# Kernel optimization log

Measured on AMD Instinct MI355X. Metric: run time of the kernel, lower is better.

## Reference

```python
import jax, jax.numpy as jnp
import numpy as np

# Config mirrors init_kwargs
D_IN, D_OUT, HEADS, SEQ, BATCH = 1024, 64, 16, 2048, 2


def setup_inputs() -> dict:
    key = jax.random.key(0)
    kx, kq, kk, kv = jax.random.split(key, 4)
    scale = 1.0 / np.sqrt(D_IN)
    x = jax.random.normal(kx, (BATCH, SEQ, D_IN), dtype=jnp.float32)
    # Stacked per-head projection weights, [H, d_in, d_out] (qkv_bias=False)
    Wq = jax.random.normal(kq, (HEADS, D_IN, D_OUT), dtype=jnp.float32) * scale
    Wk = jax.random.normal(kk, (HEADS, D_IN, D_OUT), dtype=jnp.float32) * scale
    Wv = jax.random.normal(kv, (HEADS, D_IN, D_OUT), dtype=jnp.float32) * scale
    return {"x": x, "Wq": Wq, "Wk": Wk, "Wv": Wv}


def reference(x, Wq, Wk, Wv):
    # x: [B, S, d_in]; W*: [H, d_in, d_out]
    q = jnp.einsum("bsd,hde->bhse", x, Wq)
    k = jnp.einsum("bsd,hde->bhse", x, Wk)
    v = jnp.einsum("bsd,hde->bhse", x, Wv)
    scores = jnp.einsum("bhse,bhte->bhst", q, k) / jnp.sqrt(
        jnp.asarray(D_OUT, dtype=q.dtype)
    )
    S = x.shape[1]
    causal = jnp.tril(jnp.ones((S, S), dtype=bool))  # [S, S]
    scores = jnp.where(causal[None, None], scores, -jnp.inf)
    attn = jax.nn.softmax(scores, axis=-1)  # dropout=0.0 (eval)
    ctx = jnp.einsum("bhst,bhte->bhse", attn, v)  # [B, H, S, d_out]
    # concat heads on last dim -> [B, S, H*d_out]
    B, H, S2, E = ctx.shape
    return jnp.transpose(ctx, (0, 2, 1, 3)).reshape(B, S2, H * E)
```

## Files before the change

kernel.cpp:

```cpp
#include <hip/hip_runtime.h>
#include <hip/hip_bf16.h>
#include <math.h>

#define BATCH 2
#define SEQ   2048
#define DIN   1024
#define HEADS 16
#define EDIM  64

#define NX   (BATCH*SEQ*DIN)
#define NW   (3*HEADS*DIN*EDIM)
#define NQKV (BATCH*HEADS*SEQ*EDIM)

#define QSCALE 0.18033688011112042f

typedef __attribute__((ext_vector_type(8))) short short8;
typedef __attribute__((ext_vector_type(4))) float f32x4;

static __device__ __forceinline__ ushort f2bf(float f) {
    __hip_bfloat16 h = __float2bfloat16(f);
    return *reinterpret_cast<ushort*>(&h);
}
static __device__ __forceinline__ float bf2f(ushort u) {
    uint v = (uint)u << 16;
    return *reinterpret_cast<float*>(&v);
}

static __device__ __forceinline__ void gload16(const void* g, void* l) {
    void* gv = const_cast<void*>(g);
    __builtin_amdgcn_global_load_lds(
        (__attribute__((address_space(1))) void*)gv,
        (__attribute__((address_space(3))) void*)l,
        16, 0, 0);
}

static __device__ __forceinline__ void barrier_fenced() {
    asm volatile("" ::: "memory");
    __builtin_amdgcn_s_barrier();
    asm volatile("" ::: "memory");
}

__constant__ int FT_IT[24]  = {15,15, 7,14,14,13,13, 6,12,12,11,11, 5,10,10, 9, 9, 4, 8, 8, 3, 2, 1, 0};
__constant__ int FT_K0[24]  = { 0,16, 0, 0,15, 0,14, 0, 0,13, 0,12, 0, 0,11, 0,10, 0, 0, 9, 0, 0, 0, 0};
__constant__ int FT_CNT[24] = {16,16,16,15,15,14,14,14,13,13,12,12,12,11,11,10,10,10, 9, 9, 8, 6, 4, 2};
__constant__ int FT_SL[24]  = {14,15,-1,12,13,10,11,-1, 8, 9, 6, 7,-1, 4, 5, 2, 3,-1, 0, 1,-1,-1,-1,-1};

__global__ __launch_bounds__(256) void prep(
    const float* __restrict__ x, const float* __restrict__ Wq,
    const float* __restrict__ Wk, const float* __restrict__ Wv,
    ushort* __restrict__ xb, ushort* __restrict__ wt)
{
    const int t = threadIdx.x;
    if (blockIdx.x < 1024) {
        const int v0 = blockIdx.x * 256 + t;
#pragma unroll
        for (int i = 0; i < 4; ++i) {
            int i4 = (v0 + i * 262144) * 4;
            float4 f = *(const float4*)(x + i4);
            ushort4 o;
            o.x = f2bf(f.x); o.y = f2bf(f.y); o.z = f2bf(f.z); o.w = f2bf(f.w);
            *(ushort4*)(xb + i4) = o;
        }
    } else {
        const int bid = blockIdx.x - 1024;
        const int dt  = bid & 15;
        const int h   = (bid >> 4) & 15;
        const int mat = bid >> 8;

        const float* W = (mat == 0) ? Wq : (mat == 1) ? Wk : Wv;
        const float* src = W + ((size_t)h * DIN + dt * 64) * EDIM;
        ushort* dst = wt + ((size_t)(mat * HEADS + h) * EDIM) * DIN + dt * 64;

        __shared__ ushort T[64][68];
#pragma unroll
        for (int i = 0; i < 16; ++i) {
            int v = t + i * 256;
            int d = v >> 6, e = v & 63;
            T[d][e] = f2bf(src[(size_t)d * EDIM + e]);
        }
        __syncthreads();
#pragma unroll
        for (int i = 0; i < 4; ++i) {
            int v = t + i * 256;
            int e = v >> 4, d4 = (v & 15) << 2;
            ushort4 ov;
            ov.x = T[d4 + 0][e]; ov.y = T[d4 + 1][e];
            ov.z = T[d4 + 2][e]; ov.w = T[d4 + 3][e];
            *(ushort4*)&dst[(size_t)e * DIN + d4] = ov;
        }
    }
}

__global__ __launch_bounds__(256) void qkv_gemm(
    const ushort* __restrict__ xb, const ushort* __restrict__ wt,
    ushort* __restrict__ qkv)
{
    const int bid = blockIdx.x;
    const int xcd = bid & 7;
    const int idx = bid >> 3;
    const int mt  = (xcd >> 1) * 8 + idx / 12;
    const int nt  = (xcd & 1) * 12 + idx % 12;
    const int m0 = mt * 128, n0 = nt * 128;
    const int b  = mt >> 4;

    __shared__ ushort As[2][128][64];
    __shared__ ushort Bs[2][128][64];

    const int t    = threadIdx.x;
    const int lane = t & 63;
    const int w    = t >> 6;
    const int wr   = w >> 1, wc = w & 1;
    const int fr   = lane & 15;
    const int fk   = (lane >> 4) * 8;
    const int rg   = (lane >> 4) * 4;
    const int sw   = (fr & 7) << 3;

    const ushort* xbase = xb + (size_t)m0 * DIN;
    const ushort* wbase = wt + (size_t)n0 * DIN;

    const int lrow = lane >> 3;
    const int lcol = ((lane & 7) ^ (lane >> 3)) << 3;

#define STAGE(buf, k0)                                                          \
    {                                                                           \
        _Pragma("unroll")                                                       \
        for (int j = 0; j < 4; ++j) {                                           \
            const int c = w * 4 + j;                                            \
            gload16(&xbase[(size_t)(c * 8 + lrow) * DIN + (k0) + lcol], &As[buf][c * 8][0]); \
            gload16(&wbase[(size_t)(c * 8 + lrow) * DIN + (k0) + lcol], &Bs[buf][c * 8][0]); \
        }                                                                       \
    }

    f32x4 acc[4][4];
#pragma unroll
    for (int i = 0; i < 4; ++i)
#pragma unroll
        for (int j = 0; j < 4; ++j) acc[i][j] = (f32x4)0.f;

    STAGE(0, 0);
    STAGE(1, 64);

    short8 a[4][2], bfr[4][2];

#define LOAD_FRAGS(cur)                                                         \
    {                                                                           \
        _Pragma("unroll")                                                       \
        for (int rb = 0; rb < 4; ++rb)                                          \
            _Pragma("unroll")                                                   \
            for (int kk = 0; kk < 2; ++kk) {                                    \
                a[rb][kk]   = *(const short8*)&As[cur][wr * 64 + rb * 16 + fr][(kk * 32 + fk) ^ sw]; \
                bfr[rb][kk] = *(const short8*)&Bs[cur][wc * 64 + rb * 16 + fr][(kk * 32 + fk) ^ sw]; \
            }                                                                   \
    }

#define DO_MFMA()                                                               \
    {                                                                           \
        _Pragma("unroll")                                                       \
        for (int kk = 0; kk < 2; ++kk)                                          \
            _Pragma("unroll")                                                   \
            for (int rb = 0; rb < 4; ++rb)                                      \
                _Pragma("unroll")                                               \
                for (int cf = 0; cf < 4; ++cf)                                  \
                    acc[rb][cf] = __builtin_amdgcn_mfma_f32_16x16x32_bf16(a[rb][kk], bfr[cf][kk], acc[rb][cf], 0, 0, 0); \
    }

    for (int kt = 0; kt < 15; ++kt) {
        const int cur = kt & 1;

        asm volatile("s_waitcnt vmcnt(8)" ::: "memory");
        __builtin_amdgcn_sched_barrier(0);
        barrier_fenced();

        LOAD_FRAGS(cur);

        asm volatile("s_waitcnt lgkmcnt(0)" ::: "memory");
        __builtin_amdgcn_sched_barrier(0);
        barrier_fenced();

        if (kt <= 13) STAGE(cur, (kt + 2) * 64);

        DO_MFMA();
    }
    {
        asm volatile("s_waitcnt vmcnt(0)" ::: "memory");
        __builtin_amdgcn_sched_barrier(0);
        barrier_fenced();
        LOAD_FRAGS(1);
        DO_MFMA();
    }
#undef STAGE
#undef LOAD_FRAGS
#undef DO_MFMA

    const int hg  = nt * 2 + wc;
    const int mat = hg >> 4;
    const int h   = hg & 15;
    const int s0  = (m0 & 2047) + wr * 64;
    if (mat < 2) {
        const float sc = (mat == 0) ? QSCALE : 1.0f;
        ushort* dst = qkv + (size_t)mat * NQKV
                    + ((size_t)((b * HEADS + h) * SEQ) + s0) * EDIM;
#pragma unroll
        for (int rb = 0; rb < 4; ++rb)
#pragma unroll
            for (int cf = 0; cf < 4; ++cf)
#pragma unroll
                for (int i = 0; i < 4; ++i)
                    dst[(size_t)(rb * 16 + rg + i) * EDIM + cf * 16 + fr] = f2bf(acc[rb][cf][i] * sc);
    } else {
        ushort* vtb = qkv + (size_t)2 * NQKV + ((size_t)(b * HEADS + h) * EDIM) * SEQ;
#pragma unroll
        for (int rb = 0; rb < 4; ++rb)
#pragma unroll
            for (int cf = 0; cf < 4; ++cf) {
                ushort4 ov;
                ov.x = f2bf(acc[rb][cf][0]); ov.y = f2bf(acc[rb][cf][1]);
                ov.z = f2bf(acc[rb][cf][2]); ov.w = f2bf(acc[rb][cf][3]);
                *(ushort4*)&vtb[(size_t)(cf * 16 + fr) * SEQ + s0 + rb * 16 + rg] = ov;
            }
    }
}

__global__ __launch_bounds__(512) void flash_part(
    const ushort* __restrict__ q, const ushort* __restrict__ k,
    const ushort* __restrict__ vt, float* __restrict__ out,
    ushort* __restrict__ pO, float* __restrict__ pl)
{
    const int bid  = blockIdx.x;
    const int item = bid >> 5;
    const int bh   = bid & 31;
    const int b    = bh >> 4;
    const int h    = bh & 15;
    const int it   = FT_IT[item];
    const int k0t  = FT_K0[item];
    const int cnt  = FT_CNT[item];
    const int slot = FT_SL[item];

    const ushort* Qb  = q  + ((size_t)((b * HEADS + h) * SEQ) + it * 128) * EDIM;
    const ushort* Kb  = k  + ((size_t)((b * HEADS + h) * SEQ)) * EDIM;
    const ushort* Vtb = vt + ((size_t)((b * HEADS + h) * EDIM)) * SEQ;

    __shared__ ushort Ks_[2][64][64];
    __shared__ ushort Vs_[2][64][64];
    __shared__ ushort Ps_[8][16][72];

    const int t    = threadIdx.x;
    const int lane = t & 63;
    const int w    = t >> 6;
    const int fr   = lane & 15;
    const int fk   = (lane >> 4) * 8;
    const int rg   = (lane >> 4) * 4;
    const int sw   = (fr & 7) << 3;

    const int srow8 = lane >> 3;
    const int sunit = (lane & 7) ^ srow8;

#define FSTAGE(buf, tile)                                                      \
    {                                                                          \
        gload16(&Kb[(size_t)((tile) * 64 + w * 8 + srow8) * EDIM + sunit * 8], \
                &Ks_[buf][w * 8][0]);                                          \
        gload16(&Vtb[(size_t)(w * 8 + srow8) * SEQ + (tile) * 64 + sunit * 8], \
                &Vs_[buf][w * 8][0]);                                          \
    }

    const int wrow0 = it * 128 + w * 16;
    const int lastT = wrow0 >> 6;
    const int qrow  = wrow0 + fr;

    short8 qf[2];
#pragma unroll
    for (int kk = 0; kk < 2; ++kk)
        qf[kk] = *(const short8*)&Qb[(size_t)(w * 16 + fr) * EDIM + kk * 32 + fk];
    asm volatile("s_waitcnt vmcnt(0)" ::: "memory");
    __builtin_amdgcn_sched_barrier(0);

    f32x4 o_[4];
#pragma unroll
    for (int cf = 0; cf < 4; ++cf) o_[cf] = (f32x4)0.f;
    float lpart = 0.f;

    FSTAGE(0, k0t);

    for (int ktl = 0; ktl < cnt; ++ktl) {
        const int cur  = ktl & 1;
        const int kt_g = k0t + ktl;

        asm volatile("s_waitcnt vmcnt(0)" ::: "memory");
        __builtin_amdgcn_sched_barrier(0);
        barrier_fenced();

        if (ktl + 1 < cnt) FSTAGE(cur ^ 1, k0t + ktl + 1);

        if (kt_g <= lastT) {
            f32x4 s[4];
#pragma unroll
            for (int cf = 0; cf < 4; ++cf) s[cf] = (f32x4)0.f;
#pragma unroll
            for (int cf = 0; cf < 4; ++cf)
#pragma unroll
                for (int kk = 0; kk < 2; ++kk) {
                    short8 kf = *(const short8*)&Ks_[cur][cf * 16 + fr][(kk * 32 + fk) ^ sw];
                    s[cf] = __builtin_amdgcn_mfma_f32_16x16x32_bf16(kf, qf[kk], s[cf], 0, 0, 0);
                }

            if (kt_g == lastT) {
#pragma unroll
                for (int cf = 0; cf < 4; ++cf)
#pragma unroll
                    for (int i = 0; i < 4; ++i) {
                        int kpos = kt_g * 64 + cf * 16 + rg + i;
                        if (kpos > qrow) s[cf][i] = -1e30f;
                    }
            }

            float ls = 0.f;
#pragma unroll
            for (int cf = 0; cf < 4; ++cf) {
                float p0 = __builtin_amdgcn_exp2f(s[cf][0]);
                float p1 = __builtin_amdgcn_exp2f(s[cf][1]);
                float p2 = __builtin_amdgcn_exp2f(s[cf][2]);
                float p3 = __builtin_amdgcn_exp2f(s[cf][3]);
                ls += (p0 + p1) + (p2 + p3);
                uint2 pk;
                pk.x = (uint)f2bf(p0) | ((uint)f2bf(p1) << 16);
                pk.y = (uint)f2bf(p2) | ((uint)f2bf(p3) << 16);
                *(uint2*)&Ps_[w][fr][cf * 16 + rg] = pk;
            }
            lpart += ls;

            short8 pf[2];
#pragma unroll
            for (int kb = 0; kb < 2; ++kb)
                pf[kb] = *(const short8*)&Ps_[w][fr][kb * 32 + fk];
#pragma unroll
            for (int cf = 0; cf < 4; ++cf)
#pragma unroll
                for (int kb = 0; kb < 2; ++kb) {
                    short8 vf = *(const short8*)&Vs_[cur][cf * 16 + fr][(kb * 32 + fk) ^ sw];
                    o_[cf] = __builtin_amdgcn_mfma_f32_16x16x32_bf16(vf, pf[kb], o_[cf], 0, 0, 0);
                }
        }
    }
#undef FSTAGE

    float ls = lpart;
    ls += __shfl_xor(ls, 16);
    ls += __shfl_xor(ls, 32);

    if (slot < 0) {
        const float inv = 1.f / ls;
        float* rowp = out + ((size_t)(b * SEQ + qrow)) * (HEADS * EDIM) + h * EDIM;
#pragma unroll
        for (int cf = 0; cf < 4; ++cf) {
            f32x4 ov = o_[cf] * inv;
            *(f32x4*)&rowp[cf * 16 + rg] = ov;
        }
    } else {
        ushort* po = pO + (((size_t)bh * 16 + slot) * 128 + (w * 16 + fr)) * 64;
#pragma unroll
        for (int cf = 0; cf < 4; ++cf) {
            ushort4 ov;
            ov.x = f2bf(o_[cf][0]); ov.y = f2bf(o_[cf][1]);
            ov.z = f2bf(o_[cf][2]); ov.w = f2bf(o_[cf][3]);
            *(ushort4*)&po[cf * 16 + rg] = ov;
        }
        if ((lane >> 4) == 0)
            pl[((size_t)bh * 16 + slot) * 128 + (w * 16 + fr)] = ls;
    }
}

__global__ __launch_bounds__(256) void combine(
    const ushort* __restrict__ pO, const float* __restrict__ pl,
    float* __restrict__ out)
{
    const int bid = blockIdx.x;
    const int bh  = bid & 31;
    const int b   = bh >> 4;
    const int h   = bh & 15;
    const int it8 = bid >> 5;
    const int it  = 8 + it8;

    const ushort* p0 = pO + ((size_t)bh * 16 + it8 * 2) * (128 * 64);
    const ushort* p1 = p0 + 128 * 64;
    const float*  l0 = pl + ((size_t)bh * 16 + it8 * 2) * 128;
    const float*  l1 = l0 + 128;

    const int t  = threadIdx.x;
    const int rr = t >> 6;
    const int e  = t & 63;

    for (int rb = 0; rb < 32; ++rb) {
        int row = rb * 4 + rr;
        float l = l0[row] + l1[row];
        float o = bf2f(p0[row * 64 + e]) + bf2f(p1[row * 64 + e]);
        out[((size_t)(b * SEQ + it * 128 + row)) * (HEADS * EDIM) + h * EDIM + e] = o / l;
    }
}

extern "C" void kernel_launch(void* const* d_in, const int* in_sizes, int n_in,
                              void* d_out, int out_size, void* d_ws, size_t ws_size,
                              hipStream_t stream) {
    const float* x  = (const float*)d_in[0];
    const float* Wq = (const float*)d_in[1];
    const float* Wk = (const float*)d_in[2];
    const float* Wv = (const float*)d_in[3];
    float* out = (float*)d_out;

    ushort* xb  = (ushort*)d_ws;
    ushort* wt  = xb + NX;
    ushort* qkv = wt + NW;
    ushort* pO  = qkv + (size_t)3 * NQKV;
    float*  pl  = (float*)(pO + (size_t)32 * 16 * 128 * 64);

    prep<<<1792, 256, 0, stream>>>(x, Wq, Wk, Wv, xb, wt);
    qkv_gemm<<<768, 256, 0, stream>>>(xb, wt, qkv);
    flash_part<<<768, 512, 0, stream>>>(
        qkv, qkv + NQKV, qkv + (size_t)2 * NQKV, out, pO, pl);
    combine<<<256, 256, 0, stream>>>(pO, pl, out);
}
```

Baseline: 81.43 us.

## Give each flash-attention wave two 16-row query tiles, halving block size

The flash_part kernel now runs 4 waves of 64 threads per block instead of 8. Each wave handles 32 query rows as two 16-row sub-tiles (A and B), so every K and V fragment read from shared memory feeds twice as many MFMAs. This cuts LDS read traffic per unit of math and halves the number of waves doing staging and barriers per block. In exchange, accumulator and score register use per wave roughly doubles, and fewer waves per block means less latency hiding unless occupancy rises.

```diff
diff --git a/kernel.cpp b/kernel.cpp
--- a/kernel.cpp
+++ b/kernel.cpp
@@ -221,7 +221,7 @@
     }
 }
 
-__global__ __launch_bounds__(512) void flash_part(
+__global__ __launch_bounds__(256) void flash_part(
     const ushort* __restrict__ q, const ushort* __restrict__ k,
     const ushort* __restrict__ vt, float* __restrict__ out,
     ushort* __restrict__ pO, float* __restrict__ pl)
@@ -242,7 +242,7 @@
 
     __shared__ ushort Ks_[2][64][64];
     __shared__ ushort Vs_[2][64][64];
-    __shared__ ushort Ps_[8][16][72];
+    __shared__ ushort Ps_[4][32][72];
 
     const int t    = threadIdx.x;
     const int lane = t & 63;
@@ -255,29 +255,36 @@
     const int srow8 = lane >> 3;
     const int sunit = (lane & 7) ^ srow8;
 
-#define FSTAGE(buf, tile)                                                      \
-    {                                                                          \
-        gload16(&Kb[(size_t)((tile) * 64 + w * 8 + srow8) * EDIM + sunit * 8], \
-                &Ks_[buf][w * 8][0]);                                          \
-        gload16(&Vtb[(size_t)(w * 8 + srow8) * SEQ + (tile) * 64 + sunit * 8], \
-                &Vs_[buf][w * 8][0]);                                          \
-    }
-
-    const int wrow0 = it * 128 + w * 16;
+#define FSTAGE(buf, tile)                                                        \
+    {                                                                            \
+        gload16(&Kb[(size_t)((tile) * 64 + w * 16 + srow8) * EDIM + sunit * 8],  \
+                &Ks_[buf][w * 16][0]);                                           \
+        gload16(&Kb[(size_t)((tile) * 64 + w * 16 + 8 + srow8) * EDIM + sunit * 8], \
+                &Ks_[buf][w * 16 + 8][0]);                                       \
+        gload16(&Vtb[(size_t)(w * 16 + srow8) * SEQ + (tile) * 64 + sunit * 8],  \
+                &Vs_[buf][w * 16][0]);                                           \
+        gload16(&Vtb[(size_t)(w * 16 + 8 + srow8) * SEQ + (tile) * 64 + sunit * 8], \
+                &Vs_[buf][w * 16 + 8][0]);                                       \
+    }
+
+    const int wrow0 = it * 128 + w * 32;
     const int lastT = wrow0 >> 6;
-    const int qrow  = wrow0 + fr;
-
-    short8 qf[2];
-#pragma unroll
-    for (int kk = 0; kk < 2; ++kk)
-        qf[kk] = *(const short8*)&Qb[(size_t)(w * 16 + fr) * EDIM + kk * 32 + fk];
+    const int qrowA = wrow0 + fr;
+    const int qrowB = wrow0 + 16 + fr;
+
+    short8 qfA[2], qfB[2];
+#pragma unroll
+    for (int kk = 0; kk < 2; ++kk) {
+        qfA[kk] = *(const short8*)&Qb[(size_t)(w * 32 + fr) * EDIM + kk * 32 + fk];
+        qfB[kk] = *(const short8*)&Qb[(size_t)(w * 32 + 16 + fr) * EDIM + kk * 32 + fk];
+    }
     asm volatile("s_waitcnt vmcnt(0)" ::: "memory");
     __builtin_amdgcn_sched_barrier(0);
 
-    f32x4 o_[4];
-#pragma unroll
-    for (int cf = 0; cf < 4; ++cf) o_[cf] = (f32x4)0.f;
-    float lpart = 0.f;
+    f32x4 oA[4], oB[4];
+#pragma unroll
+    for (int cf = 0; cf < 4; ++cf) { oA[cf] = (f32x4)0.f; oB[cf] = (f32x4)0.f; }
+    float lpA = 0.f, lpB = 0.f;
 
     FSTAGE(0, k0t);
 
@@ -292,16 +299,18 @@
         if (ktl + 1 < cnt) FSTAGE(cur ^ 1, k0t + ktl + 1);
 
         if (kt_g <= lastT) {
-            f32x4 s[4];
-#pragma unroll
-            for (int cf = 0; cf < 4; ++cf) s[cf] = (f32x4)0.f;
-#pragma unroll
-            for (int cf = 0; cf < 4; ++cf)
-#pragma unroll
-                for (int kk = 0; kk < 2; ++kk) {
-                    short8 kf = *(const short8*)&Ks_[cur][cf * 16 + fr][(kk * 32 + fk) ^ sw];
-                    s[cf] = __builtin_amdgcn_mfma_f32_16x16x32_bf16(kf, qf[kk], s[cf], 0, 0, 0);
-                }
+            f32x4 sA[4], sB[4];
+#pragma unroll
+            for (int cf = 0; cf < 4; ++cf) { sA[cf] = (f32x4)0.f; sB[cf] = (f32x4)0.f; }
+#pragma unroll
+            for (int cf = 0; cf < 4; ++cf) {
+                short8 kf0 = *(const short8*)&Ks_[cur][cf * 16 + fr][(fk) ^ sw];
+                short8 kf1 = *(const short8*)&Ks_[cur][cf * 16 + fr][(32 + fk) ^ sw];
+                sA[cf] = __builtin_amdgcn_mfma_f32_16x16x32_bf16(kf0, qfA[0], sA[cf], 0, 0, 0);
+                sA[cf] = __builtin_amdgcn_mfma_f32_16x16x32_bf16(kf1, qfA[1], sA[cf], 0, 0, 0);
+                sB[cf] = __builtin_amdgcn_mfma_f32_16x16x32_bf16(kf0, qfB[0], sB[cf], 0, 0, 0);
+                sB[cf] = __builtin_amdgcn_mfma_f32_16x16x32_bf16(kf1, qfB[1], sB[cf], 0, 0, 0);
+            }
 
             if (kt_g == lastT) {
 #pragma unroll
@@ -309,63 +318,87 @@
 #pragma unroll
                     for (int i = 0; i < 4; ++i) {
                         int kpos = kt_g * 64 + cf * 16 + rg + i;
-                        if (kpos > qrow) s[cf][i] = -1e30f;
+                        if (kpos > qrowA) sA[cf][i] = -1e30f;
+                        if (kpos > qrowB) sB[cf][i] = -1e30f;
                     }
             }
 
-            float ls = 0.f;
+            float lsA = 0.f, lsB = 0.f;
 #pragma unroll
             for (int cf = 0; cf < 4; ++cf) {
-                float p0 = __builtin_amdgcn_exp2f(s[cf][0]);
-                float p1 = __builtin_amdgcn_exp2f(s[cf][1]);
-                float p2 = __builtin_amdgcn_exp2f(s[cf][2]);
-                float p3 = __builtin_amdgcn_exp2f(s[cf][3]);
-                ls += (p0 + p1) + (p2 + p3);
-                uint2 pk;
-                pk.x = (uint)f2bf(p0) | ((uint)f2bf(p1) << 16);
-                pk.y = (uint)f2bf(p2) | ((uint)f2bf(p3) << 16);
-                *(uint2*)&Ps_[w][fr][cf * 16 + rg] = pk;
+                float a0 = __builtin_amdgcn_exp2f(sA[cf][0]);
+                float a1 = __builtin_amdgcn_exp2f(sA[cf][1]);
+                float a2 = __builtin_amdgcn_exp2f(sA[cf][2]);
+                float a3 = __builtin_amdgcn_exp2f(sA[cf][3]);
+                lsA += (a0 + a1) + (a2 + a3);
+                uint2 pka;
+                pka.x = (uint)f2bf(a0) | ((uint)f2bf(a1) << 16);
+                pka.y = (uint)f2bf(a2) | ((uint)f2bf(a3) << 16);
+                *(uint2*)&Ps_[w][fr][cf * 16 + rg] = pka;
+                float b0 = __builtin_amdgcn_exp2f(sB[cf][0]);
+                float b1 = __builtin_amdgcn_exp2f(sB[cf][1]);
+                float b2 = __builtin_amdgcn_exp2f(sB[cf][2]);
+                float b3 = __builtin_amdgcn_exp2f(sB[cf][3]);
+                lsB += (b0 + b1) + (b2 + b3);
+                uint2 pkb;
+                pkb.x = (uint)f2bf(b0) | ((uint)f2bf(b1) << 16);
+                pkb.y = (uint)f2bf(b2) | ((uint)f2bf(b3) << 16);
+                *(uint2*)&Ps_[w][16 + fr][cf * 16 + rg] = pkb;
             }
-            lpart += ls;
-
-            short8 pf[2];
-#pragma unroll
-            for (int kb = 0; kb < 2; ++kb)
-                pf[kb] = *(const short8*)&Ps_[w][fr][kb * 32 + fk];
-#pragma unroll
-            for (int cf = 0; cf < 4; ++cf)
-#pragma unroll
-                for (int kb = 0; kb < 2; ++kb) {
-                    short8 vf = *(const short8*)&Vs_[cur][cf * 16 + fr][(kb * 32 + fk) ^ sw];
-                    o_[cf] = __builtin_amdgcn_mfma_f32_16x16x32_bf16(vf, pf[kb], o_[cf], 0, 0, 0);
-                }
+            lpA += lsA;
+            lpB += lsB;
+
+            short8 pfA0 = *(const short8*)&Ps_[w][fr][fk];
+            short8 pfA1 = *(const short8*)&Ps_[w][fr][32 + fk];
+            short8 pfB0 = *(const short8*)&Ps_[w][16 + fr][fk];
+            short8 pfB1 = *(const short8*)&Ps_[w][16 + fr][32 + fk];
+#pragma unroll
+            for (int cf = 0; cf < 4; ++cf) {
+                short8 vf0 = *(const short8*)&Vs_[cur][cf * 16 + fr][(fk) ^ sw];
+                short8 vf1 = *(const short8*)&Vs_[cur][cf * 16 + fr][(32 + fk) ^ sw];
+                oA[cf] = __builtin_amdgcn_mfma_f32_16x16x32_bf16(vf0, pfA0, oA[cf], 0, 0, 0);
+                oA[cf] = __builtin_amdgcn_mfma_f32_16x16x32_bf16(vf1, pfA1, oA[cf], 0, 0, 0);
+                oB[cf] = __builtin_amdgcn_mfma_f32_16x16x32_bf16(vf0, pfB0, oB[cf], 0, 0, 0);
+                oB[cf] = __builtin_amdgcn_mfma_f32_16x16x32_bf16(vf1, pfB1, oB[cf], 0, 0, 0);
+            }
         }
     }
 #undef FSTAGE
 
-    float ls = lpart;
-    ls += __shfl_xor(ls, 16);
-    ls += __shfl_xor(ls, 32);
+    float lA = lpA;
+    lA += __shfl_xor(lA, 16);
+    lA += __shfl_xor(lA, 32);
+    float lB = lpB;
+    lB += __shfl_xor(lB, 16);
+    lB += __shfl_xor(lB, 32);
 
     if (slot < 0) {
-        const float inv = 1.f / ls;
-        float* rowp = out + ((size_t)(b * SEQ + qrow)) * (HEADS * EDIM) + h * EDIM;
+        const float invA = 1.f / lA;
+        const float invB = 1.f / lB;
+        float* rowpA = out + ((size_t)(b * SEQ + qrowA)) * (HEADS * EDIM) + h * EDIM;
+        float* rowpB = out + ((size_t)(b * SEQ + qrowB)) * (HEADS * EDIM) + h * EDIM;
 #pragma unroll
         for (int cf = 0; cf < 4; ++cf) {
-            f32x4 ov = o_[cf] * inv;
-            *(f32x4*)&rowp[cf * 16 + rg] = ov;
+            *(f32x4*)&rowpA[cf * 16 + rg] = oA[cf] * invA;
+            *(f32x4*)&rowpB[cf * 16 + rg] = oB[cf] * invB;
         }
     } else {
-        ushort* po = pO + (((size_t)bh * 16 + slot) * 128 + (w * 16 + fr)) * 64;
+        ushort* poA = pO + (((size_t)bh * 16 + slot) * 128 + (w * 32 + fr)) * 64;
+        ushort* poB = pO + (((size_t)bh * 16 + slot) * 128 + (w * 32 + 16 + fr)) * 64;
 #pragma unroll
         for (int cf = 0; cf < 4; ++cf) {
-            ushort4 ov;
-            ov.x = f2bf(o_[cf][0]); ov.y = f2bf(o_[cf][1]);
-            ov.z = f2bf(o_[cf][2]); ov.w = f2bf(o_[cf][3]);
-            *(ushort4*)&po[cf * 16 + rg] = ov;
-        }
-        if ((lane >> 4) == 0)
-            pl[((size_t)bh * 16 + slot) * 128 + (w * 16 + fr)] = ls;
+            ushort4 ovA, ovB;
+            ovA.x = f2bf(oA[cf][0]); ovA.y = f2bf(oA[cf][1]);
+            ovA.z = f2bf(oA[cf][2]); ovA.w = f2bf(oA[cf][3]);
+            *(ushort4*)&poA[cf * 16 + rg] = ovA;
+            ovB.x = f2bf(oB[cf][0]); ovB.y = f2bf(oB[cf][1]);
+            ovB.z = f2bf(oB[cf][2]); ovB.w = f2bf(oB[cf][3]);
+            *(ushort4*)&poB[cf * 16 + rg] = ovB;
+        }
+        if ((lane >> 4) == 0) {
+            pl[((size_t)bh * 16 + slot) * 128 + (w * 32 + fr)]      = lA;
+            pl[((size_t)bh * 16 + slot) * 128 + (w * 32 + 16 + fr)] = lB;
+        }
     }
 }
 
@@ -414,7 +447,7 @@
 
     prep<<<1792, 256, 0, stream>>>(x, Wq, Wk, Wv, xb, wt);
     qkv_gemm<<<768, 256, 0, stream>>>(xb, wt, qkv);
-    flash_part<<<768, 512, 0, stream>>>(
+    flash_part<<<768, 256, 0, stream>>>(
         qkv, qkv + NQKV, qkv + (size_t)2 * NQKV, out, pO, pl);
     combine<<<256, 256, 0, stream>>>(pO, pl, out);
 }
```

New measurement: 90.05 us. +10.6%, slower.

## Enlarge QKV GEMM tiles to 256x256 with 512-thread blocks

Applied to the files above, without the earlier changes.

The QKV projection GEMM moves from 128x128 tiles on 256 threads to 256x256 tiles on 512 threads, and the epilogue indexing is remapped to match. Each wave now owns a 128x64 sub-tile with fused fragment loads and MFMAs, and the next-stage prefetch is issued after compute. The goal is more data reuse per LDS and global load. The cost is a grid of only 192 blocks, fewer than the CU count, and less overlap between loads and MFMAs.

```diff
diff --git a/kernel.cpp b/kernel.cpp
--- a/kernel.cpp
+++ b/kernel.cpp
@@ -91,25 +91,25 @@
     }
 }
 
-__global__ __launch_bounds__(256) void qkv_gemm(
+__global__ __launch_bounds__(512) void qkv_gemm(
     const ushort* __restrict__ xb, const ushort* __restrict__ wt,
     ushort* __restrict__ qkv)
 {
     const int bid = blockIdx.x;
     const int xcd = bid & 7;
     const int idx = bid >> 3;
-    const int mt  = (xcd >> 1) * 8 + idx / 12;
-    const int nt  = (xcd & 1) * 12 + idx % 12;
-    const int m0 = mt * 128, n0 = nt * 128;
-    const int b  = mt >> 4;
-
-    __shared__ ushort As[2][128][64];
-    __shared__ ushort Bs[2][128][64];
+    const int mt  = (xcd >> 1) * 4 + idx / 6;
+    const int nt  = (xcd & 1) * 6 + idx % 6;
+    const int m0 = mt * 256, n0 = nt * 256;
+
+    __shared__ ushort As[2][256][64];
+    __shared__ ushort Bs[2][256][64];
 
     const int t    = threadIdx.x;
     const int lane = t & 63;
     const int w    = t >> 6;
-    const int wr   = w >> 1, wc = w & 1;
+    const int wm   = (w >> 2) * 128;
+    const int wn   = (w & 3) * 64;
     const int fr   = lane & 15;
     const int fk   = (lane >> 4) * 8;
     const int rg   = (lane >> 4) * 4;
@@ -131,37 +131,33 @@
         }                                                                       \
     }
 
-    f32x4 acc[4][4];
-#pragma unroll
-    for (int i = 0; i < 4; ++i)
+    f32x4 acc[8][4];
+#pragma unroll
+    for (int i = 0; i < 8; ++i)
 #pragma unroll
         for (int j = 0; j < 4; ++j) acc[i][j] = (f32x4)0.f;
 
     STAGE(0, 0);
     STAGE(1, 64);
 
-    short8 a[4][2], bfr[4][2];
-
-#define LOAD_FRAGS(cur)                                                         \
+#define COMPUTE(cur)                                                            \
     {                                                                           \
+        short8 bfr[4][2];                                                       \
         _Pragma("unroll")                                                       \
-        for (int rb = 0; rb < 4; ++rb)                                          \
+        for (int cf = 0; cf < 4; ++cf)                                          \
             _Pragma("unroll")                                                   \
-            for (int kk = 0; kk < 2; ++kk) {                                    \
-                a[rb][kk]   = *(const short8*)&As[cur][wr * 64 + rb * 16 + fr][(kk * 32 + fk) ^ sw]; \
-                bfr[rb][kk] = *(const short8*)&Bs[cur][wc * 64 + rb * 16 + fr][(kk * 32 + fk) ^ sw]; \
+            for (int kk = 0; kk < 2; ++kk)                                      \
+                bfr[cf][kk] = *(const short8*)&Bs[cur][wn + cf * 16 + fr][(kk * 32 + fk) ^ sw]; \
+        _Pragma("unroll")                                                       \
+        for (int rb = 0; rb < 8; ++rb) {                                        \
+            short8 a0 = *(const short8*)&As[cur][wm + rb * 16 + fr][(fk) ^ sw]; \
+            short8 a1 = *(const short8*)&As[cur][wm + rb * 16 + fr][(32 + fk) ^ sw]; \
+            _Pragma("unroll")                                                   \
+            for (int cf = 0; cf < 4; ++cf) {                                    \
+                acc[rb][cf] = __builtin_amdgcn_mfma_f32_16x16x32_bf16(a0, bfr[cf][0], acc[rb][cf], 0, 0, 0); \
+                acc[rb][cf] = __builtin_amdgcn_mfma_f32_16x16x32_bf16(a1, bfr[cf][1], acc[rb][cf], 0, 0, 0); \
             }                                                                   \
-    }
-
-#define DO_MFMA()                                                               \
-    {                                                                           \
-        _Pragma("unroll")                                                       \
-        for (int kk = 0; kk < 2; ++kk)                                          \
-            _Pragma("unroll")                                                   \
-            for (int rb = 0; rb < 4; ++rb)                                      \
-                _Pragma("unroll")                                               \
-                for (int cf = 0; cf < 4; ++cf)                                  \
-                    acc[rb][cf] = __builtin_amdgcn_mfma_f32_16x16x32_bf16(a[rb][kk], bfr[cf][kk], acc[rb][cf], 0, 0, 0); \
+        }                                                                       \
     }
 
     for (int kt = 0; kt < 15; ++kt) {
@@ -171,37 +167,34 @@
         __builtin_amdgcn_sched_barrier(0);
         barrier_fenced();
 
-        LOAD_FRAGS(cur);
+        COMPUTE(cur);
 
         asm volatile("s_waitcnt lgkmcnt(0)" ::: "memory");
         __builtin_amdgcn_sched_barrier(0);
         barrier_fenced();
 
         if (kt <= 13) STAGE(cur, (kt + 2) * 64);
-
-        DO_MFMA();
     }
     {
         asm volatile("s_waitcnt vmcnt(0)" ::: "memory");
         __builtin_amdgcn_sched_barrier(0);
         barrier_fenced();
-        LOAD_FRAGS(1);
-        DO_MFMA();
+        COMPUTE(1);
     }
 #undef STAGE
-#undef LOAD_FRAGS
-#undef DO_MFMA
-
-    const int hg  = nt * 2 + wc;
+#undef COMPUTE
+
+    const int hg  = nt * 4 + (w & 3);
     const int mat = hg >> 4;
     const int h   = hg & 15;
-    const int s0  = (m0 & 2047) + wr * 64;
+    const int b   = mt >> 3;
+    const int s0  = (m0 & 2047) + wm;
     if (mat < 2) {
         const float sc = (mat == 0) ? QSCALE : 1.0f;
         ushort* dst = qkv + (size_t)mat * NQKV
                     + ((size_t)((b * HEADS + h) * SEQ) + s0) * EDIM;
 #pragma unroll
-        for (int rb = 0; rb < 4; ++rb)
+        for (int rb = 0; rb < 8; ++rb)
 #pragma unroll
             for (int cf = 0; cf < 4; ++cf)
 #pragma unroll
@@ -210,7 +203,7 @@
     } else {
         ushort* vtb = qkv + (size_t)2 * NQKV + ((size_t)(b * HEADS + h) * EDIM) * SEQ;
 #pragma unroll
-        for (int rb = 0; rb < 4; ++rb)
+        for (int rb = 0; rb < 8; ++rb)
 #pragma unroll
             for (int cf = 0; cf < 4; ++cf) {
                 ushort4 ov;
@@ -413,7 +406,7 @@
     float*  pl  = (float*)(pO + (size_t)32 * 16 * 128 * 64);
 
     prep<<<1792, 256, 0, stream>>>(x, Wq, Wk, Wv, xb, wt);
-    qkv_gemm<<<768, 256, 0, stream>>>(xb, wt, qkv);
+    qkv_gemm<<<192, 512, 0, stream>>>(xb, wt, qkv);
     flash_part<<<768, 512, 0, stream>>>(
         qkv, qkv + NQKV, qkv + (size_t)2 * NQKV, out, pO, pl);
     combine<<<256, 256, 0, stream>>>(pO, pl, out);
```

New measurement: 85.75 us. 1.05x slower.
